# Performance work log

Measured on AMD Instinct MI355X. Metric: run time of the kernel, lower is better.

Reference implementation:

```python
import jax, jax.numpy as jnp
import numpy as np

PS = 5  # hard-coded patch size in Synthesiser3D


def _rotated_indices(nnf, h, w):
    """Replicates torch index computation. nnf: (bs, 3, h, w).
    Returns int32 row/col index grids of shape (bs, h, w, PS, PS)."""
    dt = nnf.dtype
    coords = jnp.transpose(nnf[:, :2], (0, 2, 3, 1))[:, :, :, None, None, :]   # (bs,h,w,1,1,2)
    angle = jnp.transpose(nnf[:, 2:3], (0, 2, 3, 1))[:, :, :, None, None, :]   # (bs,h,w,1,1,1)
    # torch_make_grid((PS,PS), center=True): grid[...,0] = j - PS//2 (yy), grid[...,1] = i - PS//2 (xx)
    r = jnp.arange(PS, dtype=dt) - PS // 2
    xx = jnp.broadcast_to(r[:, None], (PS, PS))  # xx[i,j] = i - 2
    yy = jnp.broadcast_to(r[None, :], (PS, PS))  # yy[i,j] = j - 2
    pi_i = yy.reshape(1, 1, 1, PS, PS, 1)  # split(...,0) = yy channel
    pi_j = xx.reshape(1, 1, 1, PS, PS, 1)
    s = jnp.sin(angle * np.pi)
    c = jnp.cos(angle * np.pi)
    iR = pi_i * s - pi_j * c
    jR = pi_i * c - pi_j * s
    pc = coords + jnp.concatenate([iR, jR], axis=-1)         # (bs,h,w,PS,PS,2)
    pi = jnp.clip(pc[..., 0], 0, h - 1).astype(jnp.int32)    # clamp then trunc (== torch .long())
    pj = jnp.clip(pc[..., 1], 0, w - 1).astype(jnp.int32)
    return pi, pj


def setup_inputs() -> dict:
    key = jax.random.key(0)
    k1, k2 = jax.random.split(key)
    bs, c, h, w = 2, 32, 256, 256
    source = jax.random.normal(k1, (bs, c, h, w), dtype=jnp.float32)
    u = jax.random.uniform(k2, (bs, 3, h, w), dtype=jnp.float32)
    # coordinate channels span the image; angle channel in [0,1) (multiplied by pi inside)
    scale = jnp.array([h - 1, w - 1, 1.0], dtype=jnp.float32).reshape(1, 3, 1, 1)
    nnf = u * scale
    return {"source": source, "nnf": nnf}


def reference(source, nnf):
    bs, c, h, w = source.shape
    pi, pj = _rotated_indices(nnf, h, w)                     # (bs,h,w,PS,PS) int32
    src = jnp.transpose(source, (0, 2, 3, 1)).reshape(bs, h * w, c)
    idx = (pi * w + pj).reshape(bs, -1)                      # flat gather indices
    g = jnp.take_along_axis(src, idx[..., None], axis=1)     # (bs, h*w*PS*PS, c)
    out = g.reshape(bs, h, w, PS * PS, c).sum(axis=3)        # sum over 5x5 patch
    return jnp.transpose(out, (0, 3, 1, 2))                  # (bs, c, h, w)
```

## Files before the change

kernel.cpp:

```cpp
#include <hip/hip_runtime.h>
#include <math.h>

#define BS 2
#define C  32
#define H  256
#define W  256
#define HW (H * W)
#define PS 5

#define PI_F 3.14159274101257324e+00f

__global__ __launch_bounds__(256) void transpose_chw_to_hwc(
    const float* __restrict__ src, float* __restrict__ dst) {
    __shared__ float lds[C][64 + 1];

    const int block = blockIdx.x;
    const int b     = block / (HW / 64);
    const int p0    = (block % (HW / 64)) * 64;
    const int tid   = threadIdx.x;
    const int px    = tid & 63;
    const int g     = tid >> 6;

    const float* sb = src + (size_t)b * C * HW;
    #pragma unroll
    for (int k = 0; k < 8; ++k) {
        const int ch = k * 4 + g;
        lds[ch][px] = sb[(size_t)ch * HW + p0 + px];
    }
    __syncthreads();

    float* db = dst + ((size_t)b * HW + p0) * C;
    #pragma unroll
    for (int k = 0; k < 8; ++k) {
        const int e  = k * 256 + tid;
        const int pl = e >> 5;
        const int ch = e & 31;
        db[e] = lds[ch][pl];
    }
}

__global__ __launch_bounds__(256) void gather_sum_t(
    const float* __restrict__ tsrc,
    const float* __restrict__ nnf,
    float* __restrict__ out) {
    const unsigned gid = blockIdx.x * 256u + threadIdx.x;
    const unsigned pix = gid >> 3;
    const unsigned k   = gid & 7u;
    const unsigned b   = pix >> 16;
    const unsigned p   = pix & 0xFFFFu;

    const float* nb = nnf + (size_t)b * 3 * HW;
    const float ci = nb[p];
    const float cj = nb[HW + p];
    const float a  = nb[2 * HW + p];

    const float arg = __fmul_rn(a, PI_F);
    const float s = sinf(arg);
    const float c = cosf(arg);

    float4 acc = make_float4(0.f, 0.f, 0.f, 0.f);
    const float4* tb = (const float4*)(tsrc + (size_t)b * HW * C) + k;

    #pragma unroll
    for (int i = 0; i < PS; ++i) {
        #pragma unroll
        for (int j = 0; j < PS; ++j) {
            const float fi = (float)(i - 2);
            const float fj = (float)(j - 2);
            const float iR = __fsub_rn(__fmul_rn(fj, s), __fmul_rn(fi, c));
            const float jR = __fsub_rn(__fmul_rn(fj, c), __fmul_rn(fi, s));
            float pr = __fadd_rn(ci, iR);
            float pc = __fadd_rn(cj, jR);
            pr = fminf(fmaxf(pr, 0.0f), (float)(H - 1));
            pc = fminf(fmaxf(pc, 0.0f), (float)(W - 1));
            const int row = (int)pr;
            const int col = (int)pc;
            const int idx = (row << 8) + col;
            const float4 v = tb[(size_t)idx * (C / 4)];
            acc.x += v.x; acc.y += v.y; acc.z += v.z; acc.w += v.w;
        }
    }

    float* ob = out + ((size_t)b * C + k * 4) * HW + p;
    ob[0]          = acc.x;
    ob[HW]         = acc.y;
    ob[2 * (size_t)HW] = acc.z;
    ob[3 * (size_t)HW] = acc.w;
}

__global__ __launch_bounds__(256) void gather_sum_direct(
    const float* __restrict__ src,
    const float* __restrict__ nnf,
    float* __restrict__ out) {
    const unsigned gid = blockIdx.x * 256u + threadIdx.x;
    const unsigned pix = gid >> 3;
    const unsigned k   = gid & 7u;
    const unsigned b   = pix >> 16;
    const unsigned p   = pix & 0xFFFFu;

    const float* nb = nnf + (size_t)b * 3 * HW;
    const float ci = nb[p];
    const float cj = nb[HW + p];
    const float a  = nb[2 * HW + p];

    const float arg = __fmul_rn(a, PI_F);
    const float s = sinf(arg);
    const float c = cosf(arg);

    float4 acc = make_float4(0.f, 0.f, 0.f, 0.f);
    const float* sb = src + ((size_t)b * C + k * 4) * HW;

    #pragma unroll
    for (int i = 0; i < PS; ++i) {
        #pragma unroll
        for (int j = 0; j < PS; ++j) {
            const float fi = (float)(i - 2);
            const float fj = (float)(j - 2);
            const float iR = __fsub_rn(__fmul_rn(fj, s), __fmul_rn(fi, c));
            const float jR = __fsub_rn(__fmul_rn(fj, c), __fmul_rn(fi, s));
            float pr = __fadd_rn(ci, iR);
            float pc = __fadd_rn(cj, jR);
            pr = fminf(fmaxf(pr, 0.0f), (float)(H - 1));
            pc = fminf(fmaxf(pc, 0.0f), (float)(W - 1));
            const int idx = (((int)pr) << 8) + (int)pc;
            acc.x += sb[idx];
            acc.y += sb[HW + idx];
            acc.z += sb[2 * HW + idx];
            acc.w += sb[3 * HW + idx];
        }
    }

    float* ob = out + ((size_t)b * C + k * 4) * HW + p;
    ob[0]          = acc.x;
    ob[HW]         = acc.y;
    ob[2 * (size_t)HW] = acc.z;
    ob[3 * (size_t)HW] = acc.w;
}

extern "C" void kernel_launch(void* const* d_in, const int* in_sizes, int n_in,
                              void* d_out, int out_size, void* d_ws, size_t ws_size,
                              hipStream_t stream) {
    const float* src = (const float*)d_in[0];
    const float* nnf = (const float*)d_in[1];
    float* out = (float*)d_out;

    const size_t need = (size_t)BS * HW * C * sizeof(float);
    if (ws_size >= need) {
        float* tsrc = (float*)d_ws;
        transpose_chw_to_hwc<<<BS * (HW / 64), 256, 0, stream>>>(src, tsrc);
        gather_sum_t<<<(BS * HW * 8) / 256, 256, 0, stream>>>(tsrc, nnf, out);
    } else {
        gather_sum_direct<<<(BS * HW * 8) / 256, 256, 0, stream>>>(src, nnf, out);
    }
}
```

Before: 101.0 us.

## Split transposed source into channel halves and pin gather blocks to XCDs

The transposed HWC buffer is split into two 16-channel halves, giving each half its own 4 MB per batch. Gather blocks are remapped so that each of the eight XCDs (block id mod 8) serves a single batch and channel-half combination. Each XCD's L2 therefore only has to hold one half-batch working set, which should cut the redundant DRAM and Infinity Fabric traffic caused by random gathers. In exchange, the nnf loads and sin/cos work are done twice per pixel. The fallback path for a small workspace is removed, so the code now assumes the workspace is large enough.

```diff
diff --git a/kernel.cpp b/kernel.cpp
--- a/kernel.cpp
+++ b/kernel.cpp
@@ -10,8 +10,10 @@
 
 #define PI_F 3.14159274101257324e+00f
 
-__global__ __launch_bounds__(256) void transpose_chw_to_hwc(
-    const float* __restrict__ src, float* __restrict__ dst) {
+#define HALF_FLOATS (BS * HW * 16)
+
+__global__ __launch_bounds__(256) void transpose_split(
+    const float* __restrict__ src, float* __restrict__ ws) {
     __shared__ float lds[C][64 + 1];
 
     const int block = blockIdx.x;
@@ -29,25 +31,34 @@
     }
     __syncthreads();
 
-    float* db = dst + ((size_t)b * HW + p0) * C;
+    float* lo = ws + ((size_t)b * HW + p0) * 16;
+    float* hi = ws + HALF_FLOATS + ((size_t)b * HW + p0) * 16;
     #pragma unroll
     for (int k = 0; k < 8; ++k) {
         const int e  = k * 256 + tid;
         const int pl = e >> 5;
         const int ch = e & 31;
-        db[e] = lds[ch][pl];
+        const int c  = ch & 15;
+        const float v = lds[ch][pl];
+        if (ch < 16) lo[pl * 16 + c] = v;
+        else         hi[pl * 16 + c] = v;
     }
 }
 
-__global__ __launch_bounds__(256) void gather_sum_t(
-    const float* __restrict__ tsrc,
+__global__ __launch_bounds__(256) void gather_sum_half(
+    const float* __restrict__ ws,
     const float* __restrict__ nnf,
     float* __restrict__ out) {
-    const unsigned gid = blockIdx.x * 256u + threadIdx.x;
-    const unsigned pix = gid >> 3;
-    const unsigned k   = gid & 7u;
-    const unsigned b   = pix >> 16;
-    const unsigned p   = pix & 0xFFFFu;
+    const unsigned blk   = blockIdx.x;
+    const unsigned xcd   = blk & 7u;
+    const unsigned combo = xcd >> 1;
+    const unsigned b     = combo >> 1;
+    const unsigned half  = combo & 1u;
+    const unsigned tile  = (xcd & 1u) * 512u + (blk >> 3);
+    const unsigned tid   = threadIdx.x;
+    const unsigned px    = tid >> 2;
+    const unsigned k     = tid & 3u;
+    const unsigned p     = tile * 64u + px;
 
     const float* nb = nnf + (size_t)b * 3 * HW;
     const float ci = nb[p];
@@ -58,9 +69,10 @@
     const float s = sinf(arg);
     const float c = cosf(arg);
 
+    const float4* tb = (const float4*)(ws + (size_t)half * HALF_FLOATS
+                                          + (size_t)b * HW * 16) + k;
+
     float4 acc = make_float4(0.f, 0.f, 0.f, 0.f);
-    const float4* tb = (const float4*)(tsrc + (size_t)b * HW * C) + k;
-
     #pragma unroll
     for (int i = 0; i < PS; ++i) {
         #pragma unroll
@@ -76,63 +88,14 @@
             const int row = (int)pr;
             const int col = (int)pc;
             const int idx = (row << 8) + col;
-            const float4 v = tb[(size_t)idx * (C / 4)];
+            const float4 v = tb[idx * 4];
             acc.x += v.x; acc.y += v.y; acc.z += v.z; acc.w += v.w;
         }
     }
 
-    float* ob = out + ((size_t)b * C + k * 4) * HW + p;
-    ob[0]          = acc.x;
-    ob[HW]         = acc.y;
-    ob[2 * (size_t)HW] = acc.z;
-    ob[3 * (size_t)HW] = acc.w;
-}
-
-__global__ __launch_bounds__(256) void gather_sum_direct(
-    const float* __restrict__ src,
-    const float* __restrict__ nnf,
-    float* __restrict__ out) {
-    const unsigned gid = blockIdx.x * 256u + threadIdx.x;
-    const unsigned pix = gid >> 3;
-    const unsigned k   = gid & 7u;
-    const unsigned b   = pix >> 16;
-    const unsigned p   = pix & 0xFFFFu;
-
-    const float* nb = nnf + (size_t)b * 3 * HW;
-    const float ci = nb[p];
-    const float cj = nb[HW + p];
-    const float a  = nb[2 * HW + p];
-
-    const float arg = __fmul_rn(a, PI_F);
-    const float s = sinf(arg);
-    const float c = cosf(arg);
-
-    float4 acc = make_float4(0.f, 0.f, 0.f, 0.f);
-    const float* sb = src + ((size_t)b * C + k * 4) * HW;
-
-    #pragma unroll
-    for (int i = 0; i < PS; ++i) {
-        #pragma unroll
-        for (int j = 0; j < PS; ++j) {
-            const float fi = (float)(i - 2);
-            const float fj = (float)(j - 2);
-            const float iR = __fsub_rn(__fmul_rn(fj, s), __fmul_rn(fi, c));
-            const float jR = __fsub_rn(__fmul_rn(fj, c), __fmul_rn(fi, s));
-            float pr = __fadd_rn(ci, iR);
-            float pc = __fadd_rn(cj, jR);
-            pr = fminf(fmaxf(pr, 0.0f), (float)(H - 1));
-            pc = fminf(fmaxf(pc, 0.0f), (float)(W - 1));
-            const int idx = (((int)pr) << 8) + (int)pc;
-            acc.x += sb[idx];
-            acc.y += sb[HW + idx];
-            acc.z += sb[2 * HW + idx];
-            acc.w += sb[3 * HW + idx];
-        }
-    }
-
-    float* ob = out + ((size_t)b * C + k * 4) * HW + p;
-    ob[0]          = acc.x;
-    ob[HW]         = acc.y;
+    float* ob = out + ((size_t)b * C + half * 16 + k * 4) * HW + p;
+    ob[0]              = acc.x;
+    ob[HW]             = acc.y;
     ob[2 * (size_t)HW] = acc.z;
     ob[3 * (size_t)HW] = acc.w;
 }
@@ -143,13 +106,8 @@
     const float* src = (const float*)d_in[0];
     const float* nnf = (const float*)d_in[1];
     float* out = (float*)d_out;
+    float* ws  = (float*)d_ws;
 
-    const size_t need = (size_t)BS * HW * C * sizeof(float);
-    if (ws_size >= need) {
-        float* tsrc = (float*)d_ws;
-        transpose_chw_to_hwc<<<BS * (HW / 64), 256, 0, stream>>>(src, tsrc);
-        gather_sum_t<<<(BS * HW * 8) / 256, 256, 0, stream>>>(tsrc, nnf, out);
-    } else {
-        gather_sum_direct<<<(BS * HW * 8) / 256, 256, 0, stream>>>(src, nnf, out);
-    }
+    transpose_split<<<BS * (HW / 64), 256, 0, stream>>>(src, ws);
+    gather_sum_half<<<4096, 256, 0, stream>>>(ws, nnf, out);
 }
```

Measured after the change: 105.4 us. +4.4%, slower.
